# Kernel optimization log

Measured on AMD Instinct MI355X. Metric: run time of the kernel, lower is better.

The kernel has to match this reference:

```python
import jax, jax.numpy as jnp
import numpy as np

S_CENTROIDS = 512
RADIUS = 0.5
NSAMPLE = 32
BN_EPS = 1e-5


def farthest_point_sample(xyz, s):
    # xyz: [B, N, 3] -> idx [B, s], deterministic start at index 0
    B, N, _ = xyz.shape

    def step(carry, _):
        dist, far = carry  # dist [B,N], far [B]
        centroid = jnp.take_along_axis(xyz, far[:, None, None], axis=1)  # [B,1,3]
        d = jnp.sum((xyz - centroid) ** 2, axis=-1)  # [B,N]
        dist = jnp.minimum(dist, d)
        nxt = jnp.argmax(dist, axis=-1).astype(jnp.int32)
        return (dist, nxt), far

    init = (jnp.full((B, N), 1e10, dtype=xyz.dtype), jnp.zeros((B,), jnp.int32))
    _, idx = jax.lax.scan(step, init, None, length=s)
    return idx.T  # [B, s]


def query_ball_point(radius, nsample, xyz, new_xyz):
    # xyz [B,N,3], new_xyz [B,S,3] -> group idx [B,S,nsample]
    B, N, _ = xyz.shape
    sqr = jnp.sum((new_xyz[:, :, None, :] - xyz[:, None, :, :]) ** 2, axis=-1)  # [B,S,N]
    gidx = jnp.where(sqr > radius * radius, N, jnp.arange(N, dtype=jnp.int32)[None, None, :])
    gidx = jnp.sort(gidx, axis=-1)[:, :, :nsample]  # closest-index-first valid ids
    first = gidx[:, :, :1]
    gidx = jnp.where(gidx == N, first, gidx)  # pad misses with first neighbor
    return gidx


def bn_relu(h, gamma, beta):
    # training-mode BatchNorm1d over (batch, length) dims of [BS, C, k]
    m = jnp.mean(h, axis=(0, 2), keepdims=True)
    v = jnp.var(h, axis=(0, 2), keepdims=True)
    hn = (h - m) / jnp.sqrt(v + BN_EPS)
    return jax.nn.relu(hn * gamma[None, :, None] + beta[None, :, None])


def setup_inputs() -> dict:
    key = jax.random.key(0)
    k1, k2, k3, k4 = jax.random.split(key, 4)
    B, N, Din, Dout = 16, 2048, 64, 128  # in_channels=2*Din=128
    x = jax.random.normal(k1, (B, Din, N), dtype=jnp.float32)
    coords = jax.random.uniform(k2, (B, N, 3), dtype=jnp.float32, minval=-1.0, maxval=1.0)
    W1 = jax.random.normal(k3, (Dout, 2 * Din), dtype=jnp.float32) * 0.05  # conv1 1x1 kernel
    W2 = jax.random.normal(k4, (Dout, Dout), dtype=jnp.float32) * 0.05    # conv2 1x1 kernel
    gamma1 = jnp.ones((Dout,), jnp.float32); beta1 = jnp.zeros((Dout,), jnp.float32)
    gamma2 = jnp.ones((Dout,), jnp.float32); beta2 = jnp.zeros((Dout,), jnp.float32)
    return {"x": x, "coords": coords, "W1": W1, "W2": W2,
            "gamma1": gamma1, "beta1": beta1, "gamma2": gamma2, "beta2": beta2}


def reference(x, coords, W1, W2, gamma1, beta1, gamma2, beta2):
    B = x.shape[0]
    feats = jnp.transpose(x, (0, 2, 1))  # [B, N, D]

    fidx = farthest_point_sample(coords, S_CENTROIDS)  # [B, s]
    bidx = jnp.arange(B)[:, None]
    new_xyz = coords[bidx, fidx]        # [B, s, 3]
    new_feat = feats[bidx, fidx]        # [B, s, D]

    gidx = query_ball_point(RADIUS, NSAMPLE, coords, new_xyz)  # [B, s, k]
    grouped = feats[jnp.arange(B)[:, None, None], gidx]        # [B, s, k, D]

    center = new_feat[:, :, None, :]
    agg = jnp.concatenate([grouped - center,
                           jnp.broadcast_to(center, grouped.shape)], axis=-1)  # [B, s, k, 2D]

    b, s, k, d = agg.shape
    h = jnp.transpose(agg, (0, 1, 3, 2)).reshape(b * s, d, k)  # [BS, 2D, k]
    h = bn_relu(jnp.einsum('bck,oc->bok', h, W1), gamma1, beta1)
    h = bn_relu(jnp.einsum('bck,oc->bok', h, W2), gamma2, beta2)
    pooled = jnp.max(h, axis=-1)                  # [BS, out]
    new_feature = jnp.transpose(pooled.reshape(b, s, -1), (0, 2, 1))  # [B, out, s]
    return new_xyz, new_feature
```

## Files before the change

kernel.cpp:

```cpp
#include <hip/hip_runtime.h>
#include <cstdint>

typedef unsigned int uint;
typedef unsigned short ushort_t;
typedef unsigned long long ull;
typedef __attribute__((ext_vector_type(8))) short bf16x8;
typedef __attribute__((ext_vector_type(4))) float f32x4;

#define B_   16
#define N_   2048
#define S_   512
#define G_   8192
#define DIN  64
#define DOUT 128
#define K_   32
#define ATS  136
#define ATS1 72

__device__ __forceinline__ uint bf16b(float f) {
  uint u = __float_as_uint(f);
  return (u + 0x7fffu + ((u >> 16) & 1u)) >> 16;
}
__device__ __forceinline__ float bf2f(uint b) { return __uint_as_float(b << 16); }

template<int CTRL, int RM>
__device__ __forceinline__ ull dpp_max_step(ull x) {
  uint lo = (uint)x, hi = (uint)(x >> 32);
  uint nlo = (uint)__builtin_amdgcn_update_dpp((int)lo, (int)lo, CTRL, RM, 0xf, true);
  uint nhi = (uint)__builtin_amdgcn_update_dpp((int)hi, (int)hi, CTRL, RM, 0xf, true);
  ull y = ((ull)nhi << 32) | (ull)nlo;
  return x > y ? x : y;
}
__device__ __forceinline__ ull umax64(ull a, ull b) { return a > b ? a : b; }

__global__ __launch_bounds__(512) void fps_kernel(const float* __restrict__ coords,
                                                  int* __restrict__ fidx,
                                                  float* __restrict__ out_xyz) {
  int b = blockIdx.x;
  const float* cb = coords + (size_t)b * (N_ * 3);
  __shared__ float sptx[N_], spty[N_], sptz[N_];
  __shared__ ull   skey[2][8];
  __shared__ int   sfar[S_];
  int tid = threadIdx.x, wid = tid >> 6;
  float px[4], py[4], pz[4], dist[4];
  uint nidx[4];
  int j0 = tid * 4;
  for (int j = tid; j < N_; j += 512) {
    sptx[j] = cb[3 * j]; spty[j] = cb[3 * j + 1]; sptz[j] = cb[3 * j + 2];
  }
#pragma unroll
  for (int i = 0; i < 4; ++i) {
    px[i] = cb[3 * (j0 + i)]; py[i] = cb[3 * (j0 + i) + 1]; pz[i] = cb[3 * (j0 + i) + 2];
    dist[i] = 1e10f;
    nidx[i] = ~(uint)(j0 + i);
  }
  float cx = cb[0], cy = cb[1], cz = cb[2];
  uint far = 0;
  __syncthreads();
  for (int s = 0; s < S_; ++s) {
    if (tid == 0) sfar[s] = (int)far;
    ull best = 0;
#pragma unroll
    for (int i = 0; i < 4; ++i) {
      float dx = __fsub_rn(px[i], cx);
      float dy = __fsub_rn(py[i], cy);
      float dz = __fsub_rn(pz[i], cz);
      float d = __fadd_rn(__fadd_rn(__fmul_rn(dx, dx), __fmul_rn(dy, dy)), __fmul_rn(dz, dz));
      float nd = fminf(dist[i], d);
      dist[i] = nd;
      ull p = ((ull)__float_as_uint(nd) << 32) | (ull)nidx[i];
      best = best > p ? best : p;
    }
    best = dpp_max_step<0x111, 0xf>(best);
    best = dpp_max_step<0x112, 0xf>(best);
    best = dpp_max_step<0x114, 0xf>(best);
    best = dpp_max_step<0x118, 0xf>(best);
    best = dpp_max_step<0x142, 0xa>(best);
    best = dpp_max_step<0x143, 0xc>(best);
    int pb = s & 1;
    if ((tid & 63) == 63) skey[pb][wid] = best;
    __syncthreads();
    ull k0 = skey[pb][0], k1 = skey[pb][1], k2 = skey[pb][2], k3 = skey[pb][3];
    ull k4 = skey[pb][4], k5 = skey[pb][5], k6 = skey[pb][6], k7 = skey[pb][7];
    ull a0 = umax64(k0, k1), a1 = umax64(k2, k3), a2 = umax64(k4, k5), a3 = umax64(k6, k7);
    ull kw = umax64(umax64(a0, a1), umax64(a2, a3));
    far = ~(uint)kw;
    cx = sptx[far]; cy = spty[far]; cz = sptz[far];
  }
  __syncthreads();
  if (tid < S_) {
    int f = sfar[tid];
    fidx[b * S_ + tid] = f;
    int o = (b * S_ + tid) * 3;
    out_xyz[o] = sptx[f]; out_xyz[o + 1] = spty[f]; out_xyz[o + 2] = sptz[f];
  }
}

__global__ __launch_bounds__(256) void ball_kernel(const float* __restrict__ coords,
                                                   const int* __restrict__ fidx,
                                                   int* __restrict__ gidx) {
  int lane = threadIdx.x & 63;
  int g = __builtin_amdgcn_readfirstlane(blockIdx.x * 4 + (threadIdx.x >> 6));
  int b = g >> 9;
  const float* cb = coords + (size_t)b * (N_ * 3);
  int nf = fidx[g];
  float cx = cb[3 * nf], cy = cb[3 * nf + 1], cz = cb[3 * nf + 2];
  int* out = gidx + g * K_;
  int cnt = 0, first = 0;
  bool hasfirst = false;
  for (int base = 0; base < N_; base += 64) {
    int j = base + lane;
    float dx = __fsub_rn(cb[3 * j], cx);
    float dy = __fsub_rn(cb[3 * j + 1], cy);
    float dz = __fsub_rn(cb[3 * j + 2], cz);
    float d = __fadd_rn(__fadd_rn(__fmul_rn(dx, dx), __fmul_rn(dy, dy)), __fmul_rn(dz, dz));
    bool in = (d <= 0.25f);
    ull m = __ballot(in);
    if (in) {
      int pos = cnt + __popcll(m & ((1ull << lane) - 1ull));
      if (pos < K_) out[pos] = j;
    }
    if (!hasfirst && m) { first = base + (__ffsll((long long)m) - 1); hasfirst = true; }
    cnt += __popcll(m);
    if (cnt >= K_) break;
  }
  if (cnt < K_) {
    for (int p = cnt + lane; p < K_; p += 64) out[p] = first;
  }
}

__global__ __launch_bounds__(256) void prep_kernel(const float* __restrict__ W1,
                                                   const float* __restrict__ W2,
                                                   ushort_t* __restrict__ Bp1,
                                                   ushort_t* __restrict__ Bpd,
                                                   ushort_t* __restrict__ Bp2) {
  int i = blockIdx.x * 256 + threadIdx.x;
  int j2 = i & 7, l = (i >> 3) & 63;
  {
    int kc = (i >> 9) & 3, nt = i >> 11;
    int o2 = nt * 16 + (l & 15);
    int c2 = kc * 32 + ((l >> 4) * 8) + j2;
    Bp2[i] = (ushort_t)bf16b(W2[o2 * 128 + c2]);
  }
  if (i < 8192) {
    int kc = (i >> 9) & 1, nt = (i >> 10) & 7;
    int o2 = nt * 16 + (l & 15);
    int c2 = kc * 32 + ((l >> 4) * 8) + j2;
    float wa = W1[o2 * 128 + c2];
    float wb = W1[o2 * 128 + 64 + c2];
    Bp1[i] = (ushort_t)bf16b(wa);
    Bpd[i] = (ushort_t)bf16b(wb - wa);
  }
}

__global__ __launch_bounds__(256) void gemm1_kernel(const float* __restrict__ x,
    const int* __restrict__ fidx, const int* __restrict__ gidx,
    const ushort_t* __restrict__ Bp1, const ushort_t* __restrict__ Bpd,
    ushort_t* __restrict__ h1T, float* __restrict__ psum, float* __restrict__ psq) {
  __shared__ ushort_t xgT[4][32 * ATS1];
  __shared__ float sctr[4][DIN];
  int tid = threadIdx.x;
  int lane = tid & 63, wid = tid >> 6;
  int g = __builtin_amdgcn_readfirstlane(blockIdx.x * 4 + wid);
  int b = g >> 9;
  const float* xb = x + (size_t)b * (DIN * N_);
  int nf = fidx[g];
  sctr[wid][lane] = xb[(size_t)lane * N_ + nf];
  int kk = lane & 31, ch = lane >> 5;
  int gik = gidx[g * K_ + kk];
  ushort_t* xw = xgT[wid];
#pragma unroll
  for (int cc = 0; cc < 32; ++cc) {
    int c = ch * 32 + cc;
    xw[kk * ATS1 + c] = (ushort_t)bf16b(xb[(size_t)c * N_ + gik]);
  }
  __syncthreads();
  int l15 = lane & 15, r8 = (lane >> 4) * 8;
  f32x4 acc[2][8];
#pragma unroll
  for (int nt = 0; nt < 8; ++nt) acc[0][nt] = (f32x4){0.f, 0.f, 0.f, 0.f};
#pragma unroll
  for (int kc = 0; kc < 2; ++kc) {
    union { bf16x8 v; ushort_t u[8]; } cu;
#pragma unroll
    for (int j = 0; j < 8; ++j) cu.u[j] = (ushort_t)bf16b(sctr[wid][kc * 32 + r8 + j]);
#pragma unroll
    for (int nt = 0; nt < 8; ++nt) {
      bf16x8 bf = *(const bf16x8*)(Bpd + ((nt * 2 + kc) * 64 + lane) * 8);
      acc[0][nt] = __builtin_amdgcn_mfma_f32_16x16x32_bf16(cu.v, bf, acc[0][nt], 0, 0, 0);
    }
  }
#pragma unroll
  for (int nt = 0; nt < 8; ++nt) acc[1][nt] = acc[0][nt];
#pragma unroll
  for (int kc = 0; kc < 2; ++kc) {
    bf16x8 afrag[2];
#pragma unroll
    for (int mt = 0; mt < 2; ++mt)
      afrag[mt] = *(const bf16x8*)(xw + (mt * 16 + l15) * ATS1 + kc * 32 + r8);
#pragma unroll
    for (int nt = 0; nt < 8; ++nt) {
      bf16x8 bf = *(const bf16x8*)(Bp1 + ((nt * 2 + kc) * 64 + lane) * 8);
      acc[0][nt] = __builtin_amdgcn_mfma_f32_16x16x32_bf16(afrag[0], bf, acc[0][nt], 0, 0, 0);
      acc[1][nt] = __builtin_amdgcn_mfma_f32_16x16x32_bf16(afrag[1], bf, acc[1][nt], 0, 0, 0);
    }
  }
#pragma unroll
  for (int nt = 0; nt < 8; ++nt) {
    float s = 0.f, q = 0.f;
#pragma unroll
    for (int mt = 0; mt < 2; ++mt)
#pragma unroll
      for (int r = 0; r < 4; ++r) { float a = acc[mt][nt][r]; s += a; q = fmaf(a, a, q); }
    s += __shfl_xor(s, 16, 64); s += __shfl_xor(s, 32, 64);
    q += __shfl_xor(q, 16, 64); q += __shfl_xor(q, 32, 64);
    if (lane < 16) {
      int o = nt * 16 + lane;
      psum[o * G_ + g] = s; psq[o * G_ + g] = q;
    }
  }
#pragma unroll
  for (int mt = 0; mt < 2; ++mt)
#pragma unroll
    for (int r = 0; r < 4; ++r) {
      int k = mt * 16 + (lane >> 4) * 4 + r;
      ushort_t* dst = h1T + (size_t)g * 4096 + k * 128 + l15;
#pragma unroll
      for (int nt = 0; nt < 8; ++nt)
        dst[nt * 16] = (ushort_t)bf16b(acc[mt][nt][r]);
    }
}

__global__ __launch_bounds__(256) void bn_finalize(const float* __restrict__ psum,
    const float* __restrict__ psq, const float* __restrict__ gamma,
    const float* __restrict__ beta, float* __restrict__ bnp) {
  int o = blockIdx.x, tid = threadIdx.x;
  double s = 0.0, q = 0.0;
  for (int g = tid; g < G_; g += 256) { s += (double)psum[o * G_ + g]; q += (double)psq[o * G_ + g]; }
  __shared__ double ss[256], qq[256];
  ss[tid] = s; qq[tid] = q; __syncthreads();
  for (int off = 128; off > 0; off >>= 1) {
    if (tid < off) { ss[tid] += ss[tid + off]; qq[tid] += qq[tid + off]; }
    __syncthreads();
  }
  if (tid == 0) {
    double n = 262144.0;
    double mean = ss[0] / n, var = qq[0] / n - mean * mean;
    float scv = (float)((double)gamma[o] / sqrt(var + 1e-5));
    bnp[2 * o] = scv;
    bnp[2 * o + 1] = (float)((double)beta[o] - mean * (double)scv);
  }
}

__global__ __launch_bounds__(256) void gemm2_kernel(const ushort_t* __restrict__ h1T,
    const ushort_t* __restrict__ Bp2, const float* __restrict__ bnp1,
    float* __restrict__ psum, float* __restrict__ psq,
    float* __restrict__ hmax, float* __restrict__ hmin) {
  __shared__ ushort_t actT[4][32 * ATS];
  int tid = threadIdx.x;
  int lane = tid & 63, wid = tid >> 6;
  int g = __builtin_amdgcn_readfirstlane(blockIdx.x * 4 + wid);
  ushort_t* aw = actT[wid];
  int c0 = (lane & 15) * 8;
  float s1[8], t1[8];
#pragma unroll
  for (int jj = 0; jj < 8; ++jj) { s1[jj] = bnp1[2 * (c0 + jj)]; t1[jj] = bnp1[2 * (c0 + jj) + 1]; }
  const uint4* src = (const uint4*)(h1T + (size_t)g * 4096);
#pragma unroll
  for (int t = 0; t < 8; ++t) {
    int idx = t * 64 + lane;
    uint4 v = src[idx];
    int k = idx >> 4;
    uint w[4] = {v.x, v.y, v.z, v.w};
    uint o4[4];
#pragma unroll
    for (int p2 = 0; p2 < 4; ++p2) {
      float a0 = fmaxf(fmaf(bf2f(w[p2] & 0xffffu), s1[2 * p2], t1[2 * p2]), 0.f);
      float a1 = fmaxf(fmaf(bf2f(w[p2] >> 16), s1[2 * p2 + 1], t1[2 * p2 + 1]), 0.f);
      o4[p2] = (bf16b(a1) << 16) | bf16b(a0);
    }
    *(uint4*)(aw + k * ATS + c0) = make_uint4(o4[0], o4[1], o4[2], o4[3]);
  }
  __syncthreads();
  f32x4 acc[2][8];
#pragma unroll
  for (int mt = 0; mt < 2; ++mt)
#pragma unroll
    for (int nt = 0; nt < 8; ++nt) acc[mt][nt] = (f32x4){0.f, 0.f, 0.f, 0.f};
#pragma unroll
  for (int kc = 0; kc < 4; ++kc) {
    bf16x8 afrag[2];
#pragma unroll
    for (int mt = 0; mt < 2; ++mt)
      afrag[mt] = *(const bf16x8*)(aw + (mt * 16 + (lane & 15)) * ATS + kc * 32 + (lane >> 4) * 8);
#pragma unroll
    for (int nt = 0; nt < 8; ++nt) {
      bf16x8 bfrag = *(const bf16x8*)(Bp2 + ((nt * 4 + kc) * 64 + lane) * 8);
      acc[0][nt] = __builtin_amdgcn_mfma_f32_16x16x32_bf16(afrag[0], bfrag, acc[0][nt], 0, 0, 0);
      acc[1][nt] = __builtin_amdgcn_mfma_f32_16x16x32_bf16(afrag[1], bfrag, acc[1][nt], 0, 0, 0);
    }
  }
#pragma unroll
  for (int nt = 0; nt < 8; ++nt) {
    float s = 0.f, q = 0.f, mx = -1e30f, mn = 1e30f;
#pragma unroll
    for (int mt = 0; mt < 2; ++mt)
#pragma unroll
      for (int r = 0; r < 4; ++r) {
        float a = acc[mt][nt][r];
        s += a; q = fmaf(a, a, q); mx = fmaxf(mx, a); mn = fminf(mn, a);
      }
    s += __shfl_xor(s, 16, 64); s += __shfl_xor(s, 32, 64);
    q += __shfl_xor(q, 16, 64); q += __shfl_xor(q, 32, 64);
    mx = fmaxf(mx, __shfl_xor(mx, 16, 64)); mx = fmaxf(mx, __shfl_xor(mx, 32, 64));
    mn = fminf(mn, __shfl_xor(mn, 16, 64)); mn = fminf(mn, __shfl_xor(mn, 32, 64));
    if (lane < 16) {
      int o = nt * 16 + lane;
      psum[o * G_ + g] = s; psq[o * G_ + g] = q;
      hmax[o * G_ + g] = mx; hmin[o * G_ + g] = mn;
    }
  }
}

__global__ __launch_bounds__(256) void pool_kernel(const float* __restrict__ hmax,
    const float* __restrict__ hmin, const float* __restrict__ bnp2,
    float* __restrict__ out) {
  int i = blockIdx.x * 256 + threadIdx.x;
  int s = i & 511;
  int o = (i >> 9) & 127;
  int b = i >> 16;
  int g = b * 512 + s;
  float scv = bnp2[2 * o], tf = bnp2[2 * o + 1];
  float v = (scv >= 0.f) ? hmax[o * G_ + g] : hmin[o * G_ + g];
  out[i] = fmaxf(fmaf(scv, v, tf), 0.f);
}

extern "C" void kernel_launch(void* const* d_in, const int* in_sizes, int n_in,
                              void* d_out, int out_size, void* d_ws, size_t ws_size,
                              hipStream_t stream) {
  const float* x      = (const float*)d_in[0];
  const float* coords = (const float*)d_in[1];
  const float* W1     = (const float*)d_in[2];
  const float* W2     = (const float*)d_in[3];
  const float* gamma1 = (const float*)d_in[4];
  const float* beta1  = (const float*)d_in[5];
  const float* gamma2 = (const float*)d_in[6];
  const float* beta2  = (const float*)d_in[7];
  float* out = (float*)d_out;
  char* ws = (char*)d_ws;
  ushort_t* h1T  = (ushort_t*)(ws);
  float* psum1 = (float*)(ws + 67108864);
  float* psq1  = (float*)(ws + 71303168);
  float* psum2 = (float*)(ws + 75497472);
  float* psq2  = (float*)(ws + 79691776);
  float* hmax  = (float*)(ws + 83886080);
  float* hmin  = (float*)(ws + 88080384);
  ushort_t* Bp1 = (ushort_t*)(ws + 92274688);
  ushort_t* Bpd = (ushort_t*)(ws + 92291072);
  ushort_t* Bp2 = (ushort_t*)(ws + 92307456);
  float* bnp1  = (float*)(ws + 92340224);
  float* bnp2  = (float*)(ws + 92341248);
  int* fidx    = (int*)(ws + 92342272);
  int* gidx    = (int*)(ws + 92375040);

  prep_kernel<<<64, 256, 0, stream>>>(W1, W2, Bp1, Bpd, Bp2);
  fps_kernel<<<16, 512, 0, stream>>>(coords, fidx, out);
  ball_kernel<<<2048, 256, 0, stream>>>(coords, fidx, gidx);
  gemm1_kernel<<<2048, 256, 0, stream>>>(x, fidx, gidx, Bp1, Bpd, h1T, psum1, psq1);
  bn_finalize<<<128, 256, 0, stream>>>(psum1, psq1, gamma1, beta1, bnp1);
  gemm2_kernel<<<2048, 256, 0, stream>>>(h1T, Bp2, bnp1, psum2, psq2, hmax, hmin);
  bn_finalize<<<128, 256, 0, stream>>>(psum2, psq2, gamma2, beta2, bnp2);
  pool_kernel<<<4096, 256, 0, stream>>>(hmax, hmin, bnp2, out + 24576);
}
```

Before: 429.6 us.

## Run farthest point sampling on a single wavefront with packed FP32 math

Rewrites the FPS kernel to use one 64-lane wavefront per batch, each lane holding 32 points in registers, removing the per-iteration block barrier and shared-memory cross-wave reduction. Distance updates use packed v_pk_add/mul_f32 instructions, and the wave argmax uses DPP plus readlane. Results are written directly each step. It trades more serial work per lane for eliminating synchronization latency on the critical serial loop.

```diff
diff --git a/kernel.cpp b/kernel.cpp
--- a/kernel.cpp
+++ b/kernel.cpp
@@ -6,6 +6,7 @@
 typedef unsigned long long ull;
 typedef __attribute__((ext_vector_type(8))) short bf16x8;
 typedef __attribute__((ext_vector_type(4))) float f32x4;
+typedef __attribute__((ext_vector_type(2))) float f32x2;
 
 #define B_   16
 #define N_   2048
@@ -31,68 +32,74 @@
   ull y = ((ull)nhi << 32) | (ull)nlo;
   return x > y ? x : y;
 }
-__device__ __forceinline__ ull umax64(ull a, ull b) { return a > b ? a : b; }
-
-__global__ __launch_bounds__(512) void fps_kernel(const float* __restrict__ coords,
-                                                  int* __restrict__ fidx,
-                                                  float* __restrict__ out_xyz) {
+
+__global__ __launch_bounds__(64) void fps_kernel(const float* __restrict__ coords,
+                                                 int* __restrict__ fidx,
+                                                 float* __restrict__ out_xyz) {
   int b = blockIdx.x;
   const float* cb = coords + (size_t)b * (N_ * 3);
-  __shared__ float sptx[N_], spty[N_], sptz[N_];
-  __shared__ ull   skey[2][8];
-  __shared__ int   sfar[S_];
-  int tid = threadIdx.x, wid = tid >> 6;
-  float px[4], py[4], pz[4], dist[4];
-  uint nidx[4];
-  int j0 = tid * 4;
-  for (int j = tid; j < N_; j += 512) {
-    sptx[j] = cb[3 * j]; spty[j] = cb[3 * j + 1]; sptz[j] = cb[3 * j + 2];
-  }
-#pragma unroll
-  for (int i = 0; i < 4; ++i) {
-    px[i] = cb[3 * (j0 + i)]; py[i] = cb[3 * (j0 + i) + 1]; pz[i] = cb[3 * (j0 + i) + 2];
-    dist[i] = 1e10f;
-    nidx[i] = ~(uint)(j0 + i);
+  __shared__ float spt[3][N_];
+  int lane = threadIdx.x;
+  f32x2 px[16], py[16], pz[16], dist[16];
+  {
+    const float4* src4 = (const float4*)cb + lane * 24;
+    float tmp[96];
+#pragma unroll
+    for (int t = 0; t < 24; ++t) {
+      float4 v = src4[t];
+      tmp[4 * t] = v.x; tmp[4 * t + 1] = v.y; tmp[4 * t + 2] = v.z; tmp[4 * t + 3] = v.w;
+    }
+#pragma unroll
+    for (int i = 0; i < 16; ++i) {
+      px[i].x = tmp[6 * i];     py[i].x = tmp[6 * i + 1]; pz[i].x = tmp[6 * i + 2];
+      px[i].y = tmp[6 * i + 3]; py[i].y = tmp[6 * i + 4]; pz[i].y = tmp[6 * i + 5];
+      dist[i].x = 1e10f; dist[i].y = 1e10f;
+    }
+#pragma unroll
+    for (int i = 0; i < 16; ++i) {
+      *(f32x2*)&spt[0][lane * 32 + 2 * i] = px[i];
+      *(f32x2*)&spt[1][lane * 32 + 2 * i] = py[i];
+      *(f32x2*)&spt[2][lane * 32 + 2 * i] = pz[i];
+    }
   }
   float cx = cb[0], cy = cb[1], cz = cb[2];
   uint far = 0;
-  __syncthreads();
+  uint jbase = (uint)lane * 32;
   for (int s = 0; s < S_; ++s) {
-    if (tid == 0) sfar[s] = (int)far;
-    ull best = 0;
-#pragma unroll
-    for (int i = 0; i < 4; ++i) {
-      float dx = __fsub_rn(px[i], cx);
-      float dy = __fsub_rn(py[i], cy);
-      float dz = __fsub_rn(pz[i], cz);
-      float d = __fadd_rn(__fadd_rn(__fmul_rn(dx, dx), __fmul_rn(dy, dy)), __fmul_rn(dz, dz));
-      float nd = fminf(dist[i], d);
-      dist[i] = nd;
-      ull p = ((ull)__float_as_uint(nd) << 32) | (ull)nidx[i];
-      best = best > p ? best : p;
-    }
+    if (lane < 3) {
+      float v = lane == 0 ? cx : (lane == 1 ? cy : cz);
+      out_xyz[(b * S_ + s) * 3 + lane] = v;
+      if (lane == 0) fidx[b * S_ + s] = (int)far;
+    }
+    f32x2 c2x = {cx, cx}, c2y = {cy, cy}, c2z = {cz, cz};
+    float bestv = -1.f; uint bestloc = 0;
+#pragma unroll
+    for (int i = 0; i < 16; ++i) {
+      f32x2 dx, dy, dz, qx, qy, qz, s1, s2;
+      asm("v_pk_add_f32 %0, %1, %2 neg_lo:[0,1] neg_hi:[0,1]" : "=v"(dx) : "v"(px[i]), "v"(c2x));
+      asm("v_pk_add_f32 %0, %1, %2 neg_lo:[0,1] neg_hi:[0,1]" : "=v"(dy) : "v"(py[i]), "v"(c2y));
+      asm("v_pk_add_f32 %0, %1, %2 neg_lo:[0,1] neg_hi:[0,1]" : "=v"(dz) : "v"(pz[i]), "v"(c2z));
+      asm("v_pk_mul_f32 %0, %1, %1" : "=v"(qx) : "v"(dx));
+      asm("v_pk_mul_f32 %0, %1, %1" : "=v"(qy) : "v"(dy));
+      asm("v_pk_mul_f32 %0, %1, %1" : "=v"(qz) : "v"(dz));
+      asm("v_pk_add_f32 %0, %1, %2" : "=v"(s1) : "v"(qx), "v"(qy));
+      asm("v_pk_add_f32 %0, %1, %2" : "=v"(s2) : "v"(s1), "v"(qz));
+      float n0 = fminf(dist[i].x, s2.x);
+      float n1 = fminf(dist[i].y, s2.y);
+      dist[i].x = n0; dist[i].y = n1;
+      bool g0 = n0 > bestv; bestv = g0 ? n0 : bestv; bestloc = g0 ? (uint)(2 * i) : bestloc;
+      bool g1 = n1 > bestv; bestv = g1 ? n1 : bestv; bestloc = g1 ? (uint)(2 * i + 1) : bestloc;
+    }
+    ull best = ((ull)__float_as_uint(bestv) << 32) | (ull)(~(jbase + bestloc));
     best = dpp_max_step<0x111, 0xf>(best);
     best = dpp_max_step<0x112, 0xf>(best);
     best = dpp_max_step<0x114, 0xf>(best);
     best = dpp_max_step<0x118, 0xf>(best);
     best = dpp_max_step<0x142, 0xa>(best);
     best = dpp_max_step<0x143, 0xc>(best);
-    int pb = s & 1;
-    if ((tid & 63) == 63) skey[pb][wid] = best;
-    __syncthreads();
-    ull k0 = skey[pb][0], k1 = skey[pb][1], k2 = skey[pb][2], k3 = skey[pb][3];
-    ull k4 = skey[pb][4], k5 = skey[pb][5], k6 = skey[pb][6], k7 = skey[pb][7];
-    ull a0 = umax64(k0, k1), a1 = umax64(k2, k3), a2 = umax64(k4, k5), a3 = umax64(k6, k7);
-    ull kw = umax64(umax64(a0, a1), umax64(a2, a3));
-    far = ~(uint)kw;
-    cx = sptx[far]; cy = spty[far]; cz = sptz[far];
-  }
-  __syncthreads();
-  if (tid < S_) {
-    int f = sfar[tid];
-    fidx[b * S_ + tid] = f;
-    int o = (b * S_ + tid) * 3;
-    out_xyz[o] = sptx[f]; out_xyz[o + 1] = spty[f]; out_xyz[o + 2] = sptz[f];
+    uint klo = (uint)__builtin_amdgcn_readlane((int)(uint)best, 63);
+    far = ~klo;
+    cx = spt[0][far]; cy = spt[1][far]; cz = spt[2][far];
   }
 }
 
@@ -364,7 +371,7 @@
   int* gidx    = (int*)(ws + 92375040);
 
   prep_kernel<<<64, 256, 0, stream>>>(W1, W2, Bp1, Bpd, Bp2);
-  fps_kernel<<<16, 512, 0, stream>>>(coords, fidx, out);
+  fps_kernel<<<16, 64, 0, stream>>>(coords, fidx, out);
   ball_kernel<<<2048, 256, 0, stream>>>(coords, fidx, gidx);
   gemm1_kernel<<<2048, 256, 0, stream>>>(x, fidx, gidx, Bp1, Bpd, h1T, psum1, psq1);
   bn_finalize<<<128, 256, 0, stream>>>(psum1, psq1, gamma1, beta1, bnp1);
```

Result: slower. 634.4 us (+47.7%).
